# Performance work log

Hardware: AMD Instinct MI355X
Metric: run time of the kernel (lower is better)

The kernel has to match this reference:

```python
import jax, jax.numpy as jnp
import numpy as np

# Module hyperparameters (from init_kwargs)
H_WEIGHT = 0.8
P = 5          # patch_size
D = 6          # patch_distance
MAD_SCALE = 0.6744897501960817  # Gaussian MAD -> sigma scale (skimage)

# db2 high-pass decomposition filter (pywt 'db2' dec_hi), used by skimage's
# estimate_sigma to extract the diagonal (HH) detail subband.
_DB2_HI = np.array([-0.48296291314469025, 0.8365163037378079,
                    -0.2241438680420134, -0.12940952255126037], dtype=np.float32)


def estimate_sigma(x):
    """Wavelet-based noise sigma estimate, mean over channels (skimage-style).
    x: (H, W, C) float. Returns scalar."""
    k = jnp.asarray(np.outer(_DB2_HI, _DB2_HI))[None, None]        # (1,1,4,4)
    xc = jnp.moveaxis(x, -1, 0)[:, None]                           # (C,1,H,W)
    xp = jnp.pad(xc, ((0, 0), (0, 0), (3, 3), (3, 3)), mode='symmetric')
    hh = jax.lax.conv_general_dilated(xp, k, (2, 2), 'VALID')      # (C,1,h,w)
    mad = jnp.median(jnp.abs(hh.reshape(hh.shape[0], -1)), axis=1)  # per-channel MAD
    return jnp.mean(mad / MAD_SCALE)


def _gauss_patch_kernel(p):
    # skimage slow-mode NLM Gaussian patch weighting, normalized to sum 1
    a = (p - 1) / 4.0
    u = jnp.arange(p, dtype=jnp.float32) - (p - 1) / 2.0
    g = jnp.exp(-(u * u) / (2.0 * a * a))
    k = jnp.outer(g, g)
    return (k / k.sum())[None, None]                               # (1,1,P,P)


def nl_means(x, h, sigma):
    """Slow-mode (exact) non-local means, multichannel, per skimage math:
    weight = exp(-max(d - 2*sigma^2, 0) / h^2), d = Gaussian-weighted mean
    squared patch difference averaged over channels."""
    H, W, C = x.shape
    r = P // 2
    pad = D + r
    xp = jnp.pad(x, ((pad, pad), (pad, pad), (0, 0)), mode='reflect')
    kern = _gauss_patch_kernel(P)
    var = 2.0 * sigma * sigma
    h2 = h * h

    # all (2D+1)^2 = 169 search offsets
    dy, dx = jnp.meshgrid(jnp.arange(-D, D + 1), jnp.arange(-D, D + 1), indexing='ij')
    offs = jnp.stack([dy.ravel(), dx.ravel()], axis=-1).astype(jnp.int32)  # (169,2)

    # reference patch neighborhood, shape (H+2r, W+2r, C)
    region1 = jax.lax.dynamic_slice(xp, (pad - r, pad - r, 0), (H + 2 * r, W + 2 * r, C))

    def body(carry, off):
        acc, wsum = carry
        oy, ox = off[0], off[1]
        region2 = jax.lax.dynamic_slice(
            xp, (pad - r + oy, pad - r + ox, 0), (H + 2 * r, W + 2 * r, C))
        diff2 = jnp.mean((region1 - region2) ** 2, axis=-1)        # (H+2r, W+2r)
        # Gaussian-weighted patch distance per output pixel -> (H, W)
        dist = jax.lax.conv_general_dilated(diff2[None, None], kern, (1, 1), 'VALID')[0, 0]
        wgt = jnp.exp(-jnp.maximum(dist - var, 0.0) / h2)
        ctr = jax.lax.dynamic_slice(xp, (pad + oy, pad + ox, 0), (H, W, C))
        return (acc + wgt[..., None] * ctr, wsum + wgt), None

    init = (jnp.zeros_like(x), jnp.zeros((H, W), x.dtype))
    (acc, wsum), _ = jax.lax.scan(jax.checkpoint(body), init, offs)
    return acc / wsum[..., None]


def setup_inputs() -> dict:
    key = jax.random.key(0)
    x = jax.random.uniform(key, (1024, 1024, 3), dtype=jnp.float32)  # image in [0,1]
    return {"x": x}


def reference(x):
    sigma = estimate_sigma(x)
    return nl_means(x, H_WEIGHT * sigma, sigma)
```

## Files before the change

### kernel.cpp

```cpp
#include <hip/hip_runtime.h>
#include <hip/hip_fp16.h>
#include <math.h>
#include <type_traits>


#define IMG   1024
#define HH_S  257
#define NBINS 4096
#define NREP  2
#define BIN_SCALE 4096.0f
#define MED_K 33025

#define TW 64
#define TH 32
#define PROWS 48
#define PCOLS 92
#define NPIX (PROWS*PCOLS)
#define PXB(r,c) (((r)+8)*PCOLS + ((c)+14))
#define DCOLS 80
#define ND 3360
#define HCOLS 76
#define NH 3192
#define NW 2888
#define NWP 1444
#define SWB(r,c) (((r)+6)*HCOLS + ((c)+6))

#define G0 0.05448868454910367f
#define G1 0.24420134203151178f
#define G2 0.40261994689466440f
#define B0 0.01816289484970122f
#define B1 0.08140044734383726f
#define B2 0.13420664896488813f

#define MAD_INV 1.4826022185056018f
#define LOG2E   1.4426950408889634f

typedef _Float16 half2v __attribute__((ext_vector_type(2)));
union PxU { uint2 u; half2v h[2]; };
union Q4  { uint4 u; half2v h[4]; };
union Q2  { uint2 u; half2v h[2]; };
#define H2(x) half2v{(_Float16)(x), (_Float16)(x)}

__global__ void wavelet_hist(const float* __restrict__ x, int* __restrict__ hist) {
    int idx = blockIdx.x * 256 + threadIdx.x;
    if (idx >= HH_S * HH_S) return;
    int* hrep = hist + (blockIdx.x & (NREP - 1)) * 3 * NBINS;
    int i = (idx / HH_S) * 2;
    int j = (idx - (idx / HH_S) * HH_S) * 2;
    const float k4[4] = {-0.48296291314469025f, 0.8365163037378079f,
                         -0.2241438680420134f, -0.12940952255126037f};
    float acc0 = 0.f, acc1 = 0.f, acc2 = 0.f;
    const bool fast = (j >= 2 && j <= 511);
#pragma unroll
    for (int a = 0; a < 4; ++a) {
        int sy = 2 * i + a - 3;
        sy = sy < 0 ? -sy - 1 : (sy >= IMG ? 2 * IMG - 1 - sy : sy);
        const float* row = x + (size_t)sy * IMG * 3;
        float r0, r1, r2;
        if (fast) {
            const float* p = row + (2 * j - 3) * 3;
            float f0 = p[0], f1 = p[1], f2 = p[2], f3 = p[3];
            float f4 = p[4], f5 = p[5], f6 = p[6], f7 = p[7];
            float f8 = p[8], f9 = p[9], f10 = p[10], f11 = p[11];
            r0 = k4[0] * f0 + k4[1] * f3 + k4[2] * f6 + k4[3] * f9;
            r1 = k4[0] * f1 + k4[1] * f4 + k4[2] * f7 + k4[3] * f10;
            r2 = k4[0] * f2 + k4[1] * f5 + k4[2] * f8 + k4[3] * f11;
        } else {
            r0 = r1 = r2 = 0.f;
#pragma unroll
            for (int b = 0; b < 4; ++b) {
                int sx = 2 * j + b - 3;
                sx = sx < 0 ? -sx - 1 : (sx >= IMG ? 2 * IMG - 1 - sx : sx);
                const float* p = row + sx * 3;
                r0 += k4[b] * p[0]; r1 += k4[b] * p[1]; r2 += k4[b] * p[2];
            }
        }
        acc0 += k4[a] * r0; acc1 += k4[a] * r1; acc2 += k4[a] * r2;
    }
    int b0 = (int)(fabsf(acc0) * BIN_SCALE); b0 = b0 > NBINS - 1 ? NBINS - 1 : b0;
    int b1 = (int)(fabsf(acc1) * BIN_SCALE); b1 = b1 > NBINS - 1 ? NBINS - 1 : b1;
    int b2 = (int)(fabsf(acc2) * BIN_SCALE); b2 = b2 > NBINS - 1 ? NBINS - 1 : b2;
    atomicAdd(&hrep[b0], 1);
    atomicAdd(&hrep[NBINS + b1], 1);
    atomicAdd(&hrep[2 * NBINS + b2], 1);
}

__global__ void sigma_scan(const int* __restrict__ hist, float* __restrict__ scal) {
    __shared__ int   wsum[16];
    __shared__ float sres[1];
    const int t = threadIdx.x;
    const int lane = t & 63, wid = t >> 6;
    const int c = blockIdx.x;
    const int* h = hist + c * NBINS;
    int cnt[4]; int tsum = 0;
#pragma unroll
    for (int b = 0; b < 4; ++b) {
        int bin = t * 4 + b, s = 0;
#pragma unroll
        for (int r = 0; r < NREP; ++r) s += h[r * 3 * NBINS + bin];
        cnt[b] = s; tsum += s;
    }
    int incl = tsum;
#pragma unroll
    for (int o = 1; o < 64; o <<= 1) {
        int v = __shfl_up(incl, o);
        if (lane >= o) incl += v;
    }
    if (lane == 63) wsum[wid] = incl;
    __syncthreads();
    if (wid == 0) {
        int v = (lane < 16) ? wsum[lane] : 0;
        int inc = v;
#pragma unroll
        for (int o = 1; o < 16; o <<= 1) {
            int u = __shfl_up(inc, o);
            if (lane >= o) inc += u;
        }
        if (lane < 16) wsum[lane] = inc - v;
    }
    __syncthreads();
    int cum = wsum[wid] + incl - tsum;
#pragma unroll
    for (int b = 0; b < 4; ++b) {
        int nc = cum + cnt[b];
        float v = (t * 4 + b + 0.5f) * (1.0f / BIN_SCALE);
        if (cum < MED_K && nc >= MED_K) sres[0] = v;
        cum = nc;
    }
    __syncthreads();
    if (t == 0) atomicAdd(&scal[0], sres[0] * (MAD_INV / 3.0f));
}

__device__ __forceinline__ float diff2(half2v a01, half2v a2, half2v b01, half2v b2) {
#if __has_builtin(__builtin_amdgcn_fdot2)
    half2v e01 = a01 - b01;
    half2v e2  = a2  - b2;
    return __builtin_amdgcn_fdot2(e01, e01,
           __builtin_amdgcn_fdot2(e2, e2, 0.f, false), false);
#else
    float e0 = (float)a01[0] - (float)b01[0];
    float e1 = (float)a01[1] - (float)b01[1];
    float e2 = (float)a2[0]  - (float)b2[0];
    return e0 * e0 + e1 * e1 + e2 * e2;
#endif
}

__device__ __forceinline__ half2v pack2(float a, float b) {
#if __has_builtin(__builtin_amdgcn_cvt_pkrtz)
    return __builtin_bit_cast(half2v, __builtin_amdgcn_cvt_pkrtz(a, b));
#else
    return half2v{(_Float16)a, (_Float16)b};
#endif
}

__launch_bounds__(512, 4)
__global__ void nlm_main(const float* __restrict__ x,
                         const float* __restrict__ scal,
                         float* __restrict__ out) {
    __shared__ __align__(16) uint2  spx[NPIX];
    __shared__ __align__(16) half2v sds[ND];
    __shared__ __align__(16) half2v shh[NH];
    __shared__ __align__(16) half2v swt[NW];

    const int tid = threadIdx.x;
    const int X0 = blockIdx.x * TW;
    const int Y0 = blockIdx.y * TH;

    for (int l = tid; l < NPIX; l += 512) {
        int rr = l / PCOLS;
        int cc = l - rr * PCOLS;
        int sy = Y0 + rr - 8;
        sy = sy < 0 ? -sy : (sy >= IMG ? 2 * IMG - 2 - sy : sy);
        int sc = X0 + cc - 14;
        sc = sc < 0 ? -sc : (sc >= IMG ? 2 * IMG - 2 - sc : sc);
        const float* p = x + ((size_t)sy * IMG + sc) * 3;
        uint2 u;
        u.x = (unsigned)__half_as_ushort(__float2half_rn(p[0])) |
              ((unsigned)__half_as_ushort(__float2half_rn(p[1])) << 16);
        u.y = (unsigned)__half_as_ushort(__float2half_rn(p[2]));
        spx[l] = u;
    }

    const float sigma = scal[0];
    const float var   = 2.0f * sigma * sigma;
    const float ih2l  = LOG2E / (0.64f * sigma * sigma);

    const int c  = tid & 63;
    const int rg = (tid >> 6) * 4;
    float accx[4] = {0, 0, 0, 0}, accy[4] = {0, 0, 0, 0};
    float accz[4] = {0, 0, 0, 0}, accw[4] = {0, 0, 0, 0};

    __syncthreads();

    half2v ctr01[7], ctr2[7];
    int    pb[7];
#pragma unroll
    for (int k = 0; k < 7; ++k) {
        int i = (k < 6 || tid < ND - 6 * 512) ? tid + k * 512 : 0;
        int dr = i / DCOLS;
        int dc = i - dr * DCOLS;
        pb[k] = dr * PCOLS + dc + 6;
        PxU p; p.u = spx[pb[k]];
        ctr01[k] = p.h[0]; ctr2[k] = p.h[1];
    }

    const half2v B0h = H2(B0), B1h = H2(B1), B2h = H2(B2);
    const half2v G0h = H2(G0), G1h = H2(G1), G2h = H2(G2);

    auto pair_body = [&](auto mtag, int oy1, int ox1, int oy2, int ox2) {
        constexpr bool MERGED = decltype(mtag)::value;
        const int d1off = oy1 * PCOLS + ox1;
        const int d2off = oy2 * PCOLS + ox2;

#pragma unroll
        for (int k = 0; k < 7; ++k) {
            if (k < 6 || tid < ND - 6 * 512) {
                PxU p1, p2;
                p1.u = spx[pb[k] + d1off];
                if constexpr (MERGED) p2.u = spx[pb[k] + d1off + 1];
                else                  p2.u = spx[pb[k] + d2off];
                float da = diff2(ctr01[k], ctr2[k], p1.h[0], p1.h[1]);
                float db = diff2(ctr01[k], ctr2[k], p2.h[0], p2.h[1]);
                sds[tid + k * 512] = pack2(da, db);
            }
        }
        __syncthreads();

        {
            int row = tid / 19, g = tid - row * 19;
            int b = row * DCOLS + 4 * g;
            Q4 a, q, o;
            a.u = *(const uint4*)&sds[b];
            q.u = *(const uint4*)&sds[b + 4];
            o.h[0] = B0h * a.h[0] + B1h * a.h[1] + B2h * a.h[2] + B1h * a.h[3] + B0h * q.h[0];
            o.h[1] = B0h * a.h[1] + B1h * a.h[2] + B2h * a.h[3] + B1h * q.h[0] + B0h * q.h[1];
            o.h[2] = B0h * a.h[2] + B1h * a.h[3] + B2h * q.h[0] + B1h * q.h[1] + B0h * q.h[2];
            o.h[3] = B0h * a.h[3] + B1h * q.h[0] + B2h * q.h[1] + B1h * q.h[2] + B0h * q.h[3];
            *(uint4*)&shh[row * HCOLS + 4 * g] = o.u;
            if (tid < 798 - 512) {
                int j2 = tid + 512;
                int row2 = j2 / 19, g2 = j2 - row2 * 19;
                int b2 = row2 * DCOLS + 4 * g2;
                a.u = *(const uint4*)&sds[b2];
                q.u = *(const uint4*)&sds[b2 + 4];
                o.h[0] = B0h * a.h[0] + B1h * a.h[1] + B2h * a.h[2] + B1h * a.h[3] + B0h * q.h[0];
                o.h[1] = B0h * a.h[1] + B1h * a.h[2] + B2h * a.h[3] + B1h * q.h[0] + B0h * q.h[1];
                o.h[2] = B0h * a.h[2] + B1h * a.h[3] + B2h * q.h[0] + B1h * q.h[1] + B0h * q.h[2];
                o.h[3] = B0h * a.h[3] + B1h * q.h[0] + B2h * q.h[1] + B1h * q.h[2] + B0h * q.h[3];
                *(uint4*)&shh[row2 * HCOLS + 4 * g2] = o.u;
            }
        }
        __syncthreads();

#pragma unroll
        for (int k = 0; k < 3; ++k) {
            int t = tid + k * 512;
            if (k < 2 || t < NWP) {
                int row = t / 38, cp = t - row * 38;
                int m = row * HCOLS + 2 * cp;
                Q2 s0, s1, s2, s3, s4, o;
                s0.u = *(const uint2*)&shh[m];
                s1.u = *(const uint2*)&shh[m + HCOLS];
                s2.u = *(const uint2*)&shh[m + 2 * HCOLS];
                s3.u = *(const uint2*)&shh[m + 3 * HCOLS];
                s4.u = *(const uint2*)&shh[m + 4 * HCOLS];
                half2v d0 = G0h * s0.h[0] + G1h * s1.h[0] + G2h * s2.h[0] + G1h * s3.h[0] + G0h * s4.h[0];
                half2v d1 = G0h * s0.h[1] + G1h * s1.h[1] + G2h * s2.h[1] + G1h * s3.h[1] + G0h * s4.h[1];
                o.h[0] = pack2(exp2f(fminf(var - (float)d0[0], 0.f) * ih2l),
                               exp2f(fminf(var - (float)d0[1], 0.f) * ih2l));
                o.h[1] = pack2(exp2f(fminf(var - (float)d1[0], 0.f) * ih2l),
                               exp2f(fminf(var - (float)d1[1], 0.f) * ih2l));
                *(uint2*)&swt[m] = o.u;
            }
        }
        __syncthreads();

#pragma unroll
        for (int j = 0; j < 4; ++j) {
            int r = rg + j;
            half2v wp = swt[SWB(r, c)];
            _Float16 wm1h, wm2h;
            PxU pa, pbx, pm1, pm2;
            if constexpr (MERGED) {
                int wmb = SWB(r - oy1, c - ox1);
                wm1h = swt[wmb][0];
                wm2h = swt[wmb - 1][1];
                int ab = PXB(r + oy1, c + ox1);
                pa.u  = spx[ab]; pbx.u = spx[ab + 1];
                int mb = PXB(r - oy1, c - ox1);
                pm1.u = spx[mb]; pm2.u = spx[mb - 1];
            } else {
                wm1h  = swt[SWB(r - oy1, c - ox1)][0];
                wm2h  = swt[SWB(r - oy2, c - ox2)][1];
                pa.u  = spx[PXB(r + oy1, c + ox1)];
                pbx.u = spx[PXB(r + oy2, c + ox2)];
                pm1.u = spx[PXB(r - oy1, c - ox1)];
                pm2.u = spx[PXB(r - oy2, c - ox2)];
            }
            float w1 = (float)wp[0], w2 = (float)wp[1];
            float f1 = (float)wm1h, f2 = (float)wm2h;
            accx[j] += w1 * (float)pa.h[0][0] + w2 * (float)pbx.h[0][0]
                     + f1 * (float)pm1.h[0][0] + f2 * (float)pm2.h[0][0];
            accy[j] += w1 * (float)pa.h[0][1] + w2 * (float)pbx.h[0][1]
                     + f1 * (float)pm1.h[0][1] + f2 * (float)pm2.h[0][1];
            accz[j] += w1 * (float)pa.h[1][0] + w2 * (float)pbx.h[1][0]
                     + f1 * (float)pm1.h[1][0] + f2 * (float)pm2.h[1][0];
            accw[j] += (w1 + w2) + (f1 + f2);
        }
    };

#pragma unroll 1
    for (int pi = 0; pi < 3; ++pi)
        pair_body(std::integral_constant<bool, true>{}, 0, 1 + 2 * pi, 0, 2 + 2 * pi);
#pragma unroll 1
    for (int oy = 1; oy <= 6; ++oy)
#pragma unroll 1
        for (int pi = 0; pi < 6; ++pi)
            pair_body(std::integral_constant<bool, true>{}, oy, -6 + 2 * pi, oy, -5 + 2 * pi);
#pragma unroll 1
    for (int p = 0; p < 3; ++p)
        pair_body(std::integral_constant<bool, false>{}, 2 * p + 1, 6, 2 * p + 2, 6);

#pragma unroll
    for (int j = 0; j < 4; ++j) {
        PxU p; p.u = spx[PXB(rg + j, c)];
        accx[j] += (float)p.h[0][0];
        accy[j] += (float)p.h[0][1];
        accz[j] += (float)p.h[1][0];
        accw[j] += 1.f;
    }

#pragma unroll
    for (int j = 0; j < 4; ++j) {
        int po = ((Y0 + rg + j) * IMG + X0 + c) * 3;
        float rw = 1.f / accw[j];
        out[po + 0] = accx[j] * rw;
        out[po + 1] = accy[j] * rw;
        out[po + 2] = accz[j] * rw;
    }
}

extern "C" void kernel_launch(void* const* d_in, const int* in_sizes, int n_in,
                              void* d_out, int out_size, void* d_ws, size_t ws_size,
                              hipStream_t stream) {
    const float* x = (const float*)d_in[0];
    float* out = (float*)d_out;
    float* scal = (float*)d_ws;
    int* hist = (int*)((char*)d_ws + 64);

    (void)hipMemsetAsync(d_ws, 0, 64 + NREP * 3 * NBINS * sizeof(int), stream);
    wavelet_hist<<<(HH_S * HH_S + 255) / 256, 256, 0, stream>>>(x, hist);
    sigma_scan<<<3, 1024, 0, stream>>>(hist, scal);
    dim3 grid(IMG / TW, IMG / TH);
    nlm_main<<<grid, 512, 0, stream>>>(x, scal, out);
}
```

Before: 228.8 us.

## Fuse sigma estimation and NLM into one cooperative kernel with grid syncs

```diff
diff --git a/kernel.cpp b/kernel.cpp
--- a/kernel.cpp
+++ b/kernel.cpp
@@ -1,7 +1,10 @@
 #include <hip/hip_runtime.h>
+#include <hip/hip_cooperative_groups.h>
 #include <hip/hip_fp16.h>
 #include <math.h>
 #include <type_traits>
+
+namespace cg = cooperative_groups;
 
 
 #define IMG   1024
@@ -41,96 +44,6 @@
 union Q2  { uint2 u; half2v h[2]; };
 #define H2(x) half2v{(_Float16)(x), (_Float16)(x)}
 
-__global__ void wavelet_hist(const float* __restrict__ x, int* __restrict__ hist) {
-    int idx = blockIdx.x * 256 + threadIdx.x;
-    if (idx >= HH_S * HH_S) return;
-    int* hrep = hist + (blockIdx.x & (NREP - 1)) * 3 * NBINS;
-    int i = (idx / HH_S) * 2;
-    int j = (idx - (idx / HH_S) * HH_S) * 2;
-    const float k4[4] = {-0.48296291314469025f, 0.8365163037378079f,
-                         -0.2241438680420134f, -0.12940952255126037f};
-    float acc0 = 0.f, acc1 = 0.f, acc2 = 0.f;
-    const bool fast = (j >= 2 && j <= 511);
-#pragma unroll
-    for (int a = 0; a < 4; ++a) {
-        int sy = 2 * i + a - 3;
-        sy = sy < 0 ? -sy - 1 : (sy >= IMG ? 2 * IMG - 1 - sy : sy);
-        const float* row = x + (size_t)sy * IMG * 3;
-        float r0, r1, r2;
-        if (fast) {
-            const float* p = row + (2 * j - 3) * 3;
-            float f0 = p[0], f1 = p[1], f2 = p[2], f3 = p[3];
-            float f4 = p[4], f5 = p[5], f6 = p[6], f7 = p[7];
-            float f8 = p[8], f9 = p[9], f10 = p[10], f11 = p[11];
-            r0 = k4[0] * f0 + k4[1] * f3 + k4[2] * f6 + k4[3] * f9;
-            r1 = k4[0] * f1 + k4[1] * f4 + k4[2] * f7 + k4[3] * f10;
-            r2 = k4[0] * f2 + k4[1] * f5 + k4[2] * f8 + k4[3] * f11;
-        } else {
-            r0 = r1 = r2 = 0.f;
-#pragma unroll
-            for (int b = 0; b < 4; ++b) {
-                int sx = 2 * j + b - 3;
-                sx = sx < 0 ? -sx - 1 : (sx >= IMG ? 2 * IMG - 1 - sx : sx);
-                const float* p = row + sx * 3;
-                r0 += k4[b] * p[0]; r1 += k4[b] * p[1]; r2 += k4[b] * p[2];
-            }
-        }
-        acc0 += k4[a] * r0; acc1 += k4[a] * r1; acc2 += k4[a] * r2;
-    }
-    int b0 = (int)(fabsf(acc0) * BIN_SCALE); b0 = b0 > NBINS - 1 ? NBINS - 1 : b0;
-    int b1 = (int)(fabsf(acc1) * BIN_SCALE); b1 = b1 > NBINS - 1 ? NBINS - 1 : b1;
-    int b2 = (int)(fabsf(acc2) * BIN_SCALE); b2 = b2 > NBINS - 1 ? NBINS - 1 : b2;
-    atomicAdd(&hrep[b0], 1);
-    atomicAdd(&hrep[NBINS + b1], 1);
-    atomicAdd(&hrep[2 * NBINS + b2], 1);
-}
-
-__global__ void sigma_scan(const int* __restrict__ hist, float* __restrict__ scal) {
-    __shared__ int   wsum[16];
-    __shared__ float sres[1];
-    const int t = threadIdx.x;
-    const int lane = t & 63, wid = t >> 6;
-    const int c = blockIdx.x;
-    const int* h = hist + c * NBINS;
-    int cnt[4]; int tsum = 0;
-#pragma unroll
-    for (int b = 0; b < 4; ++b) {
-        int bin = t * 4 + b, s = 0;
-#pragma unroll
-        for (int r = 0; r < NREP; ++r) s += h[r * 3 * NBINS + bin];
-        cnt[b] = s; tsum += s;
-    }
-    int incl = tsum;
-#pragma unroll
-    for (int o = 1; o < 64; o <<= 1) {
-        int v = __shfl_up(incl, o);
-        if (lane >= o) incl += v;
-    }
-    if (lane == 63) wsum[wid] = incl;
-    __syncthreads();
-    if (wid == 0) {
-        int v = (lane < 16) ? wsum[lane] : 0;
-        int inc = v;
-#pragma unroll
-        for (int o = 1; o < 16; o <<= 1) {
-            int u = __shfl_up(inc, o);
-            if (lane >= o) inc += u;
-        }
-        if (lane < 16) wsum[lane] = inc - v;
-    }
-    __syncthreads();
-    int cum = wsum[wid] + incl - tsum;
-#pragma unroll
-    for (int b = 0; b < 4; ++b) {
-        int nc = cum + cnt[b];
-        float v = (t * 4 + b + 0.5f) * (1.0f / BIN_SCALE);
-        if (cum < MED_K && nc >= MED_K) sres[0] = v;
-        cum = nc;
-    }
-    __syncthreads();
-    if (t == 0) atomicAdd(&scal[0], sres[0] * (MAD_INV / 3.0f));
-}
-
 __device__ __forceinline__ float diff2(half2v a01, half2v a2, half2v b01, half2v b2) {
 #if __has_builtin(__builtin_amdgcn_fdot2)
     half2v e01 = a01 - b01;
@@ -153,19 +66,8 @@
 #endif
 }
 
-__launch_bounds__(512, 4)
-__global__ void nlm_main(const float* __restrict__ x,
-                         const float* __restrict__ scal,
-                         float* __restrict__ out) {
-    __shared__ __align__(16) uint2  spx[NPIX];
-    __shared__ __align__(16) half2v sds[ND];
-    __shared__ __align__(16) half2v shh[NH];
-    __shared__ __align__(16) half2v swt[NW];
-
-    const int tid = threadIdx.x;
-    const int X0 = blockIdx.x * TW;
-    const int Y0 = blockIdx.y * TH;
-
+__device__ __forceinline__ void tile_load(const float* __restrict__ x, uint2* spx,
+                                          int tid, int X0, int Y0) {
     for (int l = tid; l < NPIX; l += 512) {
         int rr = l / PCOLS;
         int cc = l - rr * PCOLS;
@@ -180,8 +82,89 @@
         u.y = (unsigned)__half_as_ushort(__float2half_rn(p[2]));
         spx[l] = u;
     }
-
-    const float sigma = scal[0];
+}
+
+__device__ __forceinline__ void hist_accum(const float* __restrict__ x,
+                                           int* __restrict__ hist,
+                                           int gtid, int rep) {
+    if (gtid >= HH_S * HH_S * 3) return;
+    int idx = gtid / 3;
+    int c   = gtid - idx * 3;
+    int i = idx / HH_S;
+    int j = idx - i * HH_S;
+    const float k4[4] = {-0.48296291314469025f, 0.8365163037378079f,
+                         -0.2241438680420134f, -0.12940952255126037f};
+    float acc = 0.f;
+    const bool fast = (j >= 2);
+#pragma unroll
+    for (int a = 0; a < 4; ++a) {
+        int sy = 2 * i + a - 3;
+        sy = sy < 0 ? -sy - 1 : (sy >= IMG ? 2 * IMG - 1 - sy : sy);
+        const float* row = x + (size_t)sy * IMG * 3;
+        float r;
+        if (fast) {
+            const float* p = row + (2 * j - 3) * 3 + c;
+            r = k4[0] * p[0] + k4[1] * p[3] + k4[2] * p[6] + k4[3] * p[9];
+        } else {
+            r = 0.f;
+#pragma unroll
+            for (int b = 0; b < 4; ++b) {
+                int sx = 2 * j + b - 3;
+                sx = sx < 0 ? -sx - 1 : sx;
+                r += k4[b] * row[sx * 3 + c];
+            }
+        }
+        acc += k4[a] * r;
+    }
+    int b0 = (int)(fabsf(acc) * BIN_SCALE); b0 = b0 > NBINS - 1 ? NBINS - 1 : b0;
+    atomicAdd(&hist[rep * 3 * NBINS + c * NBINS + b0], 1);
+}
+
+__device__ __forceinline__ void median_scan(const int* __restrict__ hist,
+                                            float* __restrict__ scal,
+                                            int c, int tid, int* wsum) {
+    const int lane = tid & 63, wid = tid >> 6;
+    const int* h = hist + c * NBINS;
+    int cnt[8]; int tsum = 0;
+#pragma unroll
+    for (int b = 0; b < 8; ++b) {
+        int bin = tid * 8 + b, s = 0;
+#pragma unroll
+        for (int r = 0; r < NREP; ++r) s += h[r * 3 * NBINS + bin];
+        cnt[b] = s; tsum += s;
+    }
+    int incl = tsum;
+#pragma unroll
+    for (int o = 1; o < 64; o <<= 1) {
+        int v = __shfl_up(incl, o);
+        if (lane >= o) incl += v;
+    }
+    if (lane == 63) wsum[wid] = incl;
+    __syncthreads();
+    if (wid == 0) {
+        int v = (lane < 8) ? wsum[lane] : 0;
+        int inc = v;
+#pragma unroll
+        for (int o = 1; o < 8; o <<= 1) {
+            int u = __shfl_up(inc, o);
+            if (lane >= o) inc += u;
+        }
+        if (lane < 8) wsum[lane] = inc - v;
+    }
+    __syncthreads();
+    int cum = wsum[wid] + incl - tsum;
+#pragma unroll
+    for (int b = 0; b < 8; ++b) {
+        int nc = cum + cnt[b];
+        if (cum < MED_K && nc >= MED_K)
+            scal[c] = (tid * 8 + b + 0.5f) * (1.0f / BIN_SCALE);
+        cum = nc;
+    }
+}
+
+__device__ __forceinline__ void nlm_loop(float* __restrict__ out, float sigma,
+                                         uint2* spx, half2v* sds, half2v* shh,
+                                         half2v* swt, int tid, int X0, int Y0) {
     const float var   = 2.0f * sigma * sigma;
     const float ih2l  = LOG2E / (0.64f * sigma * sigma);
 
@@ -340,6 +323,144 @@
     }
 }
 
+__launch_bounds__(512, 4)
+__global__ void nlm_fused(const float* __restrict__ x, float* __restrict__ scal,
+                          int* __restrict__ hist, float* __restrict__ out) {
+    __shared__ __align__(16) uint2  spx[NPIX];
+    __shared__ __align__(16) half2v sds[ND];
+    __shared__ __align__(16) half2v shh[NH];
+    __shared__ __align__(16) half2v swt[NW];
+
+    const int tid = threadIdx.x;
+    const int bid = blockIdx.y * gridDim.x + blockIdx.x;
+    const int X0 = blockIdx.x * TW;
+    const int Y0 = blockIdx.y * TH;
+
+    hist_accum(x, hist, bid * 512 + tid, bid & (NREP - 1));
+    tile_load(x, spx, tid, X0, Y0);
+
+    cg::this_grid().sync();
+
+    if (bid < 3) median_scan(hist, scal, bid, tid, (int*)sds);
+
+    cg::this_grid().sync();
+
+    float s0 = __hip_atomic_load(&scal[0], __ATOMIC_RELAXED, __HIP_MEMORY_SCOPE_AGENT);
+    float s1 = __hip_atomic_load(&scal[1], __ATOMIC_RELAXED, __HIP_MEMORY_SCOPE_AGENT);
+    float s2 = __hip_atomic_load(&scal[2], __ATOMIC_RELAXED, __HIP_MEMORY_SCOPE_AGENT);
+    const float sigma = (s0 + s1 + s2) * (MAD_INV / 3.0f);
+
+    nlm_loop(out, sigma, spx, sds, shh, swt, tid, X0, Y0);
+}
+
+__global__ void wavelet_hist(const float* __restrict__ x, int* __restrict__ hist) {
+    int idx = blockIdx.x * 256 + threadIdx.x;
+    if (idx >= HH_S * HH_S) return;
+    int* hrep = hist + (blockIdx.x & (NREP - 1)) * 3 * NBINS;
+    int i = (idx / HH_S) * 2;
+    int j = (idx - (idx / HH_S) * HH_S) * 2;
+    const float k4[4] = {-0.48296291314469025f, 0.8365163037378079f,
+                         -0.2241438680420134f, -0.12940952255126037f};
+    float acc0 = 0.f, acc1 = 0.f, acc2 = 0.f;
+    const bool fast = (j >= 2 && j <= 511);
+#pragma unroll
+    for (int a = 0; a < 4; ++a) {
+        int sy = 2 * i + a - 3;
+        sy = sy < 0 ? -sy - 1 : (sy >= IMG ? 2 * IMG - 1 - sy : sy);
+        const float* row = x + (size_t)sy * IMG * 3;
+        float r0, r1, r2;
+        if (fast) {
+            const float* p = row + (2 * j - 3) * 3;
+            float f0 = p[0], f1 = p[1], f2 = p[2], f3 = p[3];
+            float f4 = p[4], f5 = p[5], f6 = p[6], f7 = p[7];
+            float f8 = p[8], f9 = p[9], f10 = p[10], f11 = p[11];
+            r0 = k4[0] * f0 + k4[1] * f3 + k4[2] * f6 + k4[3] * f9;
+            r1 = k4[0] * f1 + k4[1] * f4 + k4[2] * f7 + k4[3] * f10;
+            r2 = k4[0] * f2 + k4[1] * f5 + k4[2] * f8 + k4[3] * f11;
+        } else {
+            r0 = r1 = r2 = 0.f;
+#pragma unroll
+            for (int b = 0; b < 4; ++b) {
+                int sx = 2 * j + b - 3;
+                sx = sx < 0 ? -sx - 1 : (sx >= IMG ? 2 * IMG - 1 - sx : sx);
+                const float* p = row + sx * 3;
+                r0 += k4[b] * p[0]; r1 += k4[b] * p[1]; r2 += k4[b] * p[2];
+            }
+        }
+        acc0 += k4[a] * r0; acc1 += k4[a] * r1; acc2 += k4[a] * r2;
+    }
+    int b0 = (int)(fabsf(acc0) * BIN_SCALE); b0 = b0 > NBINS - 1 ? NBINS - 1 : b0;
+    int b1 = (int)(fabsf(acc1) * BIN_SCALE); b1 = b1 > NBINS - 1 ? NBINS - 1 : b1;
+    int b2 = (int)(fabsf(acc2) * BIN_SCALE); b2 = b2 > NBINS - 1 ? NBINS - 1 : b2;
+    atomicAdd(&hrep[b0], 1);
+    atomicAdd(&hrep[NBINS + b1], 1);
+    atomicAdd(&hrep[2 * NBINS + b2], 1);
+}
+
+__global__ void sigma_scan(const int* __restrict__ hist, float* __restrict__ scal) {
+    __shared__ int   wsum[16];
+    __shared__ float sres[1];
+    const int t = threadIdx.x;
+    const int lane = t & 63, wid = t >> 6;
+    const int c = blockIdx.x;
+    const int* h = hist + c * NBINS;
+    int cnt[4]; int tsum = 0;
+#pragma unroll
+    for (int b = 0; b < 4; ++b) {
+        int bin = t * 4 + b, s = 0;
+#pragma unroll
+        for (int r = 0; r < NREP; ++r) s += h[r * 3 * NBINS + bin];
+        cnt[b] = s; tsum += s;
+    }
+    int incl = tsum;
+#pragma unroll
+    for (int o = 1; o < 64; o <<= 1) {
+        int v = __shfl_up(incl, o);
+        if (lane >= o) incl += v;
+    }
+    if (lane == 63) wsum[wid] = incl;
+    __syncthreads();
+    if (wid == 0) {
+        int v = (lane < 16) ? wsum[lane] : 0;
+        int inc = v;
+#pragma unroll
+        for (int o = 1; o < 16; o <<= 1) {
+            int u = __shfl_up(inc, o);
+            if (lane >= o) inc += u;
+        }
+        if (lane < 16) wsum[lane] = inc - v;
+    }
+    __syncthreads();
+    int cum = wsum[wid] + incl - tsum;
+#pragma unroll
+    for (int b = 0; b < 4; ++b) {
+        int nc = cum + cnt[b];
+        float v = (t * 4 + b + 0.5f) * (1.0f / BIN_SCALE);
+        if (cum < MED_K && nc >= MED_K) sres[0] = v;
+        cum = nc;
+    }
+    __syncthreads();
+    if (t == 0) atomicAdd(&scal[0], sres[0] * (MAD_INV / 3.0f));
+}
+
+__launch_bounds__(512, 4)
+__global__ void nlm_main(const float* __restrict__ x,
+                         const float* __restrict__ scal,
+                         float* __restrict__ out) {
+    __shared__ __align__(16) uint2  spx[NPIX];
+    __shared__ __align__(16) half2v sds[ND];
+    __shared__ __align__(16) half2v shh[NH];
+    __shared__ __align__(16) half2v swt[NW];
+
+    const int tid = threadIdx.x;
+    const int X0 = blockIdx.x * TW;
+    const int Y0 = blockIdx.y * TH;
+
+    tile_load(x, spx, tid, X0, Y0);
+    const float sigma = scal[0];
+    nlm_loop(out, sigma, spx, sds, shh, swt, tid, X0, Y0);
+}
+
 extern "C" void kernel_launch(void* const* d_in, const int* in_sizes, int n_in,
                               void* d_out, int out_size, void* d_ws, size_t ws_size,
                               hipStream_t stream) {
@@ -349,8 +470,15 @@
     int* hist = (int*)((char*)d_ws + 64);
 
     (void)hipMemsetAsync(d_ws, 0, 64 + NREP * 3 * NBINS * sizeof(int), stream);
-    wavelet_hist<<<(HH_S * HH_S + 255) / 256, 256, 0, stream>>>(x, hist);
-    sigma_scan<<<3, 1024, 0, stream>>>(hist, scal);
+
     dim3 grid(IMG / TW, IMG / TH);
-    nlm_main<<<grid, 512, 0, stream>>>(x, scal, out);
-}
+    const float* xa = x; float* sa = scal; int* ha = hist; float* oa = out;
+    void* args[] = {(void*)&xa, (void*)&sa, (void*)&ha, (void*)&oa};
+    hipError_t e = hipLaunchCooperativeKernel((const void*)nlm_fused, grid,
+                                              dim3(512, 1, 1), args, 0, stream);
+    if (e != hipSuccess) {
+        wavelet_hist<<<(HH_S * HH_S + 255) / 256, 256, 0, stream>>>(x, hist);
+        sigma_scan<<<3, 1024, 0, stream>>>(hist, scal);
+        nlm_main<<<grid, 512, 0, stream>>>(x, scal, out);
+    }
+}
```

Result: slower. 361.6 us (+58.1%).
